# Kernel optimization log

Hardware: AMD Instinct MI355X
Metric: run time of the kernel (lower is better)

Reference implementation:

```python
import jax, jax.numpy as jnp
import numpy as np

T_IN, T_OUT, B, D, H, L = 257, 256, 256, 131, 256, 2


def lstm_cell(x, h, c, Wih, Whh, bih, bhh):
    # torch LSTMCell gate order: i, f, g, o
    z = x @ Wih.T + h @ Whh.T + bih + bhh
    i, f, g, o = jnp.split(z, 4, axis=-1)
    c_new = jax.nn.sigmoid(f) * c + jax.nn.sigmoid(i) * jnp.tanh(g)
    h_new = jax.nn.sigmoid(o) * jnp.tanh(c_new)
    return h_new, c_new


def setup_inputs() -> dict:
    key = jax.random.key(0)
    ks = jax.random.split(key, 22)
    s = 0.05  # weight scale, keeps gates in the linear-ish region
    d = {}
    d["X"] = jax.random.normal(ks[0], (T_IN, B, D), jnp.float32)
    d["Y"] = jax.random.normal(ks[1], (T_OUT, B, D), jnp.float32)
    shapes = {
        "enc_Wih0": (4 * H, D), "enc_Whh0": (4 * H, H), "enc_bih0": (4 * H,), "enc_bhh0": (4 * H,),
        "enc_Wih1": (4 * H, H), "enc_Whh1": (4 * H, H), "enc_bih1": (4 * H,), "enc_bhh1": (4 * H,),
        "dec_Wih0": (4 * H, D), "dec_Whh0": (4 * H, H), "dec_bih0": (4 * H,), "dec_bhh0": (4 * H,),
        "dec_Wih1": (4 * H, H), "dec_Whh1": (4 * H, H), "dec_bih1": (4 * H,), "dec_bhh1": (4 * H,),
        "lin_W": (D, H), "lin_b": (D,),
    }
    for i, (name, shp) in enumerate(shapes.items()):
        d[name] = jax.random.normal(ks[2 + i], shp, jnp.float32) * s
    return d


def _make_step(params, emit):
    def step(carry, x):
        hs, cs = carry
        inp = x
        new_h, new_c = [], []
        for l, (Wih, Whh, bih, bhh) in enumerate(params):
            h, c = lstm_cell(inp, hs[l], cs[l], Wih, Whh, bih, bhh)
            new_h.append(h)
            new_c.append(c)
            inp = h
        out = emit(inp) if emit is not None else None
        return (tuple(new_h), tuple(new_c)), out
    return step


def reference(X, Y, enc_Wih0, enc_Whh0, enc_bih0, enc_bhh0,
              enc_Wih1, enc_Whh1, enc_bih1, enc_bhh1,
              dec_Wih0, dec_Whh0, dec_bih0, dec_bhh0,
              dec_Wih1, dec_Whh1, dec_bih1, dec_bhh1,
              lin_W, lin_b):
    enc = [(enc_Wih0, enc_Whh0, enc_bih0, enc_bhh0),
           (enc_Wih1, enc_Whh1, enc_bih1, enc_bhh1)]
    dec = [(dec_Wih0, dec_Whh0, dec_bih0, dec_bhh0),
           (dec_Wih1, dec_Whh1, dec_bih1, dec_bhh1)]
    b = X.shape[1]
    zeros = tuple(jnp.zeros((b, H), X.dtype) for _ in range(L))
    # encoder over X[:-1]
    (hn, cn), _ = jax.lax.scan(_make_step(enc, None), (zeros, zeros), X[:-1])
    # decoder (teacher forcing): inputs are [X[-1], Y[0], ..., Y[T_out-2]]
    dec_in = jnp.concatenate([X[-1:], Y[:-1]], axis=0)
    emit = lambda h: jax.nn.log_softmax(h @ lin_W.T + lin_b, axis=-1)
    _, Ypred = jax.lax.scan(_make_step(dec, emit), (hn, cn), dec_in)
    return Ypred  # (T_out, B, out_dim) log-probabilities
```

## Files before the change

kernel.cpp:

```cpp
#include <hip/hip_runtime.h>
#include <hip/hip_bf16.h>
#include <math.h>

typedef __attribute__((ext_vector_type(8))) short short8;
typedef __attribute__((ext_vector_type(4))) float f32x4;
typedef unsigned long long u64;
typedef __attribute__((ext_vector_type(2))) unsigned long long u64x2;

#define STEPS 512
#define BB 256
#define HH 256
#define DD 131
#define XP 160
#define K0P 416
#define KS0 424
#define K1  512
#define KS1 520
#define HS0 264
#define HS1 520
#define RING 16
#define PO   8
#define NGRP 8
#define ROWS 32
#define SLOT_E (ROWS * HH)
#define RGELEM (RING * SLOT_E)
#define POISON64 0x7F807F807F807F80ull

#define OFF_W0E 0
#define OFF_W0D (OFF_W0E + 1024 * K0P)
#define OFF_W1E (OFF_W0D + 1024 * K0P)
#define OFF_W1D (OFF_W1E + 1024 * K1)
#define OFF_LW  (OFF_W1D + 1024 * K1)
#define OFF_XBF (OFF_LW + 160 * 256)
#define OFF_H0R (OFF_XBF + (size_t)STEPS * BB * XP)
#define OFF_H1R (OFF_H0R + (size_t)NGRP * RGELEM)
#define OFF_H1A (OFF_H1R + (size_t)NGRP * RGELEM)
#define OFF_BF16_END (OFF_H1A + (size_t)256 * BB * HH)

#define LDS_W_OFF  0
#define LDS_HS_OFF 66560
#define LDS_TOTAL  133120

__device__ __forceinline__ float rcp_(float x) { return __builtin_amdgcn_rcpf(x); }
__device__ __forceinline__ float fsigm(float x) { return rcp_(1.f + __expf(-x)); }
__device__ __forceinline__ float ftanh(float x) {
    float t = __expf(-2.f * fabsf(x));
    float r = (1.f - t) * rcp_(1.f + t);
    return copysignf(r, x);
}
__device__ __forceinline__ void astore(u64* p, u64 v) {
    __hip_atomic_store(p, v, __ATOMIC_RELAXED, __HIP_MEMORY_SCOPE_AGENT);
}
__device__ __forceinline__ void pload(const u64* p, u64x2& r) {
    asm volatile("global_load_dwordx4 %0, %1, off sc0 sc1" : "=v"(r) : "v"(p));
}
__device__ __forceinline__ void pll_drain() {
    asm volatile("s_waitcnt vmcnt(0)" ::: "memory");
    __builtin_amdgcn_sched_barrier(0);
}

__global__ __launch_bounds__(256) void pack_w0(const float* __restrict__ Wih,
                                               const float* __restrict__ Whh,
                                               __hip_bfloat16* __restrict__ dst) {
    int idx = blockIdx.x * 256 + threadIdx.x;
    int p = idx / K0P, k = idx - p * K0P;
    int ct = p >> 6, local = p & 63, g = local >> 4, j = local & 15;
    int orow = g * 256 + ct * 16 + j;
    float v = 0.f;
    if (k < DD) v = Wih[orow * DD + k];
    else if (k >= XP) v = Whh[orow * HH + (k - XP)];
    dst[idx] = __float2bfloat16(v);
}

__global__ __launch_bounds__(256) void pack_w1(const float* __restrict__ Wih,
                                               const float* __restrict__ Whh,
                                               __hip_bfloat16* __restrict__ dst) {
    int idx = blockIdx.x * 256 + threadIdx.x;
    int p = idx >> 9, k = idx & 511;
    int ct = p >> 6, local = p & 63, g = local >> 4, j = local & 15;
    int orow = g * 256 + ct * 16 + j;
    float v = (k < HH) ? Wih[orow * HH + k] : Whh[orow * HH + (k - HH)];
    dst[idx] = __float2bfloat16(v);
}

__global__ __launch_bounds__(256) void pack_bias(const float* __restrict__ bih,
                                                 const float* __restrict__ bhh,
                                                 float* __restrict__ dst) {
    int idx = blockIdx.x * 256 + threadIdx.x;
    if (idx < 1024) dst[idx] = bih[idx] + bhh[idx];
}

__global__ __launch_bounds__(256) void pack_xbf(const float* __restrict__ X,
                                                const float* __restrict__ Y,
                                                __hip_bfloat16* __restrict__ dst) {
    int idx = blockIdx.x * 256 + threadIdx.x;
    int kp = idx % XP;
    int rb = idx / XP;
    int b = rb & 255, s = rb >> 8;
    const float* src;
    if (s <= 256) src = X + ((size_t)s * BB + b) * DD;
    else          src = Y + ((size_t)(s - 257) * BB + b) * DD;
    dst[idx] = __float2bfloat16(kp < DD ? src[kp] : 0.f);
}

__global__ __launch_bounds__(256) void pack_linw(const float* __restrict__ linW,
                                                 __hip_bfloat16* __restrict__ dst) {
    int idx = blockIdx.x * 256 + threadIdx.x;
    int j = idx >> 8, k = idx & 255;
    dst[idx] = __float2bfloat16(j < DD ? linW[j * HH + k] : 0.f);
}

__global__ __launch_bounds__(256) void pack_linb(const float* __restrict__ linb,
                                                 float* __restrict__ dst) {
    int idx = threadIdx.x;
    if (idx < 160) dst[idx] = (idx < DD) ? linb[idx] : -1.0e30f;
}

__global__ __launch_bounds__(256) void init_rings(u64* __restrict__ rings,
                                                  int* __restrict__ acks) {
    int idx = blockIdx.x * 256 + threadIdx.x;
    if (idx < 2 * NGRP * (RGELEM / 4)) {
        int slot = (idx >> 11) & (RING - 1);
        rings[idx] = (slot == RING - 1) ? 0ull : POISON64;
    }
    if (idx < 256) acks[idx] = 0;
}

__global__ __launch_bounds__(512, 1) void lstm_persistent(
    const __hip_bfloat16* __restrict__ wsb,
    const float* __restrict__ bsum,
    __hip_bfloat16* __restrict__ h0ring,
    __hip_bfloat16* __restrict__ h1ring,
    __hip_bfloat16* __restrict__ h1all,
    int* __restrict__ acks) {
    extern __shared__ __align__(16) char lds[];
    __hip_bfloat16* Wlds = (__hip_bfloat16*)(lds + LDS_W_OFF);
    __hip_bfloat16* hst  = (__hip_bfloat16*)(lds + LDS_HS_OFF);

    const int tid = threadIdx.x;
    const int wg = blockIdx.x;
    const int xg = wg >> 5;
    const int slot_id = wg & 31;
    const int layer = slot_id >> 4;
    const int ct = slot_id & 15;
    const int lane = tid & 63;
    const int mt = tid >> 6;
    const int lrow = lane & 15;
    const int lk8 = (lane >> 4) * 8;

    const int K  = layer ? K1 : K0P;
    const int KS = layer ? KS1 : KS0;
    const int HS = layer ? HS1 : HS0;
    int* ackp = acks + xg * 32;

    auto load_w = [&](int ph2) {
        const __hip_bfloat16* src = wsb +
            (layer ? (ph2 ? OFF_W1D : OFF_W1E) : (ph2 ? OFF_W0D : OFF_W0E)) +
            (size_t)ct * 64 * K;
        const int KC = K >> 3;
        for (int e = tid; e < 64 * KC; e += 512) {
            int p = e / KC, kc = e - p * KC;
            *(short8*)&Wlds[p * KS + kc * 8] =
                *(const short8*)&src[(size_t)p * K + kc * 8];
        }
    };
    load_w(0);

    const int jcol = ct * 16 + lrow;
    float br[2][4];
    #pragma unroll
    for (int ph = 0; ph < 2; ++ph)
        #pragma unroll
        for (int g = 0; g < 4; ++g)
            br[ph][g] = bsum[ph * 2048 + layer * 1024 + g * 256 + jcol];
    f32x4 creg = {0.f, 0.f, 0.f, 0.f};

    const __hip_bfloat16* Xbf = wsb + OFF_XBF;
    __hip_bfloat16* h0g = h0ring + (size_t)xg * RGELEM;
    __hip_bfloat16* h1g = h1ring + (size_t)xg * RGELEM;
    __hip_bfloat16* ringw = layer ? h1g : h0g;
    const int arow = mt * 16 + lrow;
    __syncthreads();

    for (int s = 0; s < STEPS; ++s) {
        const int ph = s >> 8;
        const bool defer_x = (s == 256);
        f32x4 acc[4];
        short8 xv[5];

        if (tid < 128) {
            #pragma unroll
            for (int g = 0; g < 4; ++g) acc[g] = (f32x4){0.f, 0.f, 0.f, 0.f};
            if (layer == 0) {
                const short8* xp = (const short8*)
                    &Xbf[((size_t)s * BB + xg * ROWS + arow) * XP];
                #pragma unroll
                for (int kt = 0; kt < 5; ++kt) xv[kt] = xp[kt * 4 + (lk8 >> 3)];
                if (!defer_x) {
                    #pragma unroll
                    for (int kt = 0; kt < 5; ++kt)
                        #pragma unroll
                        for (int g = 0; g < 4; ++g) {
                            short8 w = *(const short8*)
                                &Wlds[(g * 16 + lrow) * KS0 + kt * 32 + lk8];
                            acc[g] = __builtin_amdgcn_mfma_f32_16x16x32_bf16(
                                xv[kt], w, acc[g], 0, 0, 0);
                        }
                }
            }
        } else {
            const int ptid = tid - 128;
            __hip_bfloat16* hs = hst + (s & 1) * 32 * HS;
            if (layer == 0) {
                const u64* src = (const u64*)(h0g +
                    (size_t)((s + RING - 1) & (RING - 1)) * SLOT_E);
                u64x2 v[3];
                unsigned pend = 0;
                #pragma unroll
                for (int i = 0; i < 3; ++i)
                    if (ptid + i * 384 < 1024) pend |= (1u << i);
                int guard = 0;
                while (pend) {
                    #pragma unroll
                    for (int i = 0; i < 3; ++i)
                        if (pend & (1u << i))
                            pload(src + 2 * (ptid + i * 384), v[i]);
                    pll_drain();
                    unsigned np = 0;
                    #pragma unroll
                    for (int i = 0; i < 3; ++i)
                        if ((pend & (1u << i)) &&
                            (((v[i][0] & 0xFFFFull) == 0x7F80ull) ||
                             ((v[i][1] & 0xFFFFull) == 0x7F80ull)))
                            np |= (1u << i);
                    pend = np;
                    if (pend && ++guard > 65536) break;
                }
                #pragma unroll
                for (int i = 0; i < 3; ++i) {
                    int q = ptid + i * 384;
                    if (q < 1024)
                        *(u64x2*)&hs[(q >> 5) * HS0 + (q & 31) * 8] = v[i];
                }
                if (ptid == 383) {
                    int tgt = 16 * (s - (PO - 1));
                    if (tgt > 0) {
                        int guard2 = 0;
                        while (__hip_atomic_load(ackp, __ATOMIC_RELAXED,
                                                 __HIP_MEMORY_SCOPE_AGENT) < tgt) {
                            __builtin_amdgcn_s_sleep(1);
                            if (++guard2 > 65536) break;
                        }
                    }
                }
            } else {
                const u64* s0 = (const u64*)(h0g +
                    (size_t)(s & (RING - 1)) * SLOT_E);
                const u64* s1 = (const u64*)(h1g +
                    (size_t)((s + RING - 1) & (RING - 1)) * SLOT_E);
                u64x2 v0[3], v1[3];
                unsigned pend = 0;
                #pragma unroll
                for (int i = 0; i < 3; ++i)
                    if (ptid + i * 384 < 1024) pend |= (0x101u << i);
                int guard = 0;
                while (pend) {
                    #pragma unroll
                    for (int i = 0; i < 3; ++i) {
                        if (pend & (1u << i))
                            pload(s0 + 2 * (ptid + i * 384), v0[i]);
                        if (pend & (0x100u << i))
                            pload(s1 + 2 * (ptid + i * 384), v1[i]);
                    }
                    pll_drain();
                    unsigned np = 0;
                    #pragma unroll
                    for (int i = 0; i < 3; ++i) {
                        if ((pend & (1u << i)) &&
                            (((v0[i][0] & 0xFFFFull) == 0x7F80ull) ||
                             ((v0[i][1] & 0xFFFFull) == 0x7F80ull)))
                            np |= (1u << i);
                        if ((pend & (0x100u << i)) &&
                            (((v1[i][0] & 0xFFFFull) == 0x7F80ull) ||
                             ((v1[i][1] & 0xFFFFull) == 0x7F80ull)))
                            np |= (0x100u << i);
                    }
                    pend = np;
                    if (pend && ++guard > 65536) break;
                }
                #pragma unroll
                for (int i = 0; i < 3; ++i) {
                    int q = ptid + i * 384;
                    if (q < 1024) {
                        *(u64x2*)&hs[(q >> 5) * HS1 + (q & 31) * 8] = v0[i];
                        *(u64x2*)&hs[(q >> 5) * HS1 + 256 + (q & 31) * 8] = v1[i];
                    }
                }
            }
        }
        __syncthreads();
        if (s == 256) { load_w(1); __syncthreads(); }

        if (tid < 128) {
            if (layer == 1 && tid == 0)
                __hip_atomic_fetch_add(ackp, 1, __ATOMIC_RELAXED,
                                       __HIP_MEMORY_SCOPE_AGENT);
            const __hip_bfloat16* hs = hst + (s & 1) * 32 * HS;
            if (layer == 0) {
                if (defer_x) {
                    #pragma unroll
                    for (int kt = 0; kt < 5; ++kt)
                        #pragma unroll
                        for (int g = 0; g < 4; ++g) {
                            short8 w = *(const short8*)
                                &Wlds[(g * 16 + lrow) * KS0 + kt * 32 + lk8];
                            acc[g] = __builtin_amdgcn_mfma_f32_16x16x32_bf16(
                                xv[kt], w, acc[g], 0, 0, 0);
                        }
                }
                #pragma unroll
                for (int kt = 0; kt < 8; ++kt) {
                    short8 a = *(const short8*)&hs[arow * HS0 + kt * 32 + lk8];
                    #pragma unroll
                    for (int g = 0; g < 4; ++g) {
                        short8 w = *(const short8*)
                            &Wlds[(g * 16 + lrow) * KS0 + (5 + kt) * 32 + lk8];
                        acc[g] = __builtin_amdgcn_mfma_f32_16x16x32_bf16(
                            a, w, acc[g], 0, 0, 0);
                    }
                }
            } else {
                #pragma unroll
                for (int kt = 0; kt < 16; ++kt) {
                    short8 a = *(const short8*)&hs[arow * HS1 + kt * 32 + lk8];
                    #pragma unroll
                    for (int g = 0; g < 4; ++g) {
                        short8 w = *(const short8*)
                            &Wlds[(g * 16 + lrow) * KS1 + kt * 32 + lk8];
                        acc[g] = __builtin_amdgcn_mfma_f32_16x16x32_bf16(
                            a, w, acc[g], 0, 0, 0);
                    }
                }
            }

            unsigned short hu[4];
            #pragma unroll
            for (int r = 0; r < 4; ++r) {
                float zi = acc[0][r] + br[ph][0];
                float zf = acc[1][r] + br[ph][1];
                float zg = acc[2][r] + br[ph][2];
                float zo = acc[3][r] + br[ph][3];
                float ig = fsigm(zi), fg = fsigm(zf), og = fsigm(zo);
                float cn = fg * creg[r] + ig * ftanh(zg);
                creg[r] = cn;
                union { __hip_bfloat16 b; unsigned short u; } cvt;
                cvt.b = __float2bfloat16(og * ftanh(cn));
                hu[r] = cvt.u;
            }

            {
                const int m = lane & 15, g16 = lane >> 4;
                const int srcbase = g16 * 16 + 4 * (m & 3);
                const int myslot = m >> 2;
                unsigned short pa = 0, pb = 0, pc = 0, pd = 0;
                #pragma unroll
                for (int rr = 0; rr < 4; ++rr) {
                    int q0 = __shfl((int)hu[rr], srcbase + 0, 64);
                    int q1 = __shfl((int)hu[rr], srcbase + 1, 64);
                    int q2 = __shfl((int)hu[rr], srcbase + 2, 64);
                    int q3 = __shfl((int)hu[rr], srcbase + 3, 64);
                    if (myslot == rr) {
                        pa = (unsigned short)q0; pb = (unsigned short)q1;
                        pc = (unsigned short)q2; pd = (unsigned short)q3;
                    }
                }
                u64 pkt = (u64)pa | ((u64)pb << 16) | ((u64)pc << 32)
                        | ((u64)pd << 48);
                const int prow = mt * 16 + g16 * 4 + myslot;
                const int pq = m & 3;
                astore((u64*)(ringw + (size_t)(s & (RING - 1)) * SLOT_E)
                       + prow * 64 + ct * 4 + pq, pkt);
                if (layer == 1 && s >= 256)
                    *(u64*)&h1all[((size_t)(s - 256) * BB + xg * ROWS + prow) * HH
                                  + ct * 16 + pq * 4] = pkt;
                astore((u64*)(ringw + (size_t)((s + PO) & (RING - 1)) * SLOT_E)
                       + prow * 64 + ct * 4 + pq, POISON64);
            }
        }
    }
}

__global__ __launch_bounds__(256) void emit_mfma(
    const __hip_bfloat16* __restrict__ h1all,
    const __hip_bfloat16* __restrict__ lW,
    const float* __restrict__ lb,
    float* __restrict__ out) {
    __shared__ float lbs[160];
    const int tid = threadIdx.x;
    const int wv = tid >> 6, lane = tid & 63;
    const int lrow = lane & 15, lk8 = (lane >> 4) * 8, crow = (lane >> 4) * 4;
    const int row0 = blockIdx.x * 64;
    if (tid < 160) lbs[tid] = lb[tid];
    __syncthreads();

    f32x4 acc[10];
    #pragma unroll
    for (int f = 0; f < 10; ++f) acc[f] = (f32x4){0.f, 0.f, 0.f, 0.f};
    const int arow = row0 + wv * 16 + lrow;
    #pragma unroll
    for (int kt = 0; kt < 8; ++kt) {
        short8 a = *reinterpret_cast<const short8*>(
            &h1all[(size_t)arow * HH + kt * 32 + lk8]);
        #pragma unroll
        for (int f = 0; f < 10; ++f) {
            short8 w = *reinterpret_cast<const short8*>(
                &lW[(size_t)(f * 16 + lrow) * HH + kt * 32 + lk8]);
            acc[f] = __builtin_amdgcn_mfma_f32_16x16x32_bf16(a, w, acc[f], 0, 0, 0);
        }
    }
    #pragma unroll
    for (int r = 0; r < 4; ++r) {
        float m = -3.0e38f;
        #pragma unroll
        for (int f = 0; f < 10; ++f) m = fmaxf(m, acc[f][r] + lbs[f * 16 + lrow]);
        #pragma unroll
        for (int d = 1; d < 16; d <<= 1) m = fmaxf(m, __shfl_xor(m, d, 64));
        float ss = 0.f;
        #pragma unroll
        for (int f = 0; f < 10; ++f) ss += __expf(acc[f][r] + lbs[f * 16 + lrow] - m);
        #pragma unroll
        for (int d = 1; d < 16; d <<= 1) ss += __shfl_xor(ss, d, 64);
        float lse = m + logf(ss);
        int grow = row0 + wv * 16 + crow + r;
        #pragma unroll
        for (int f = 0; f < 9; ++f) {
            int j = f * 16 + lrow;
            if (j < DD)
                out[(size_t)grow * DD + j] = acc[f][r] + lbs[j] - lse;
        }
    }
}

extern "C" void kernel_launch(void* const* d_in, const int* in_sizes, int n_in,
                              void* d_out, int out_size, void* d_ws, size_t ws_size,
                              hipStream_t stream) {
    const float* X     = (const float*)d_in[0];
    const float* Y     = (const float*)d_in[1];
    const float* eWih0 = (const float*)d_in[2];
    const float* eWhh0 = (const float*)d_in[3];
    const float* ebih0 = (const float*)d_in[4];
    const float* ebhh0 = (const float*)d_in[5];
    const float* eWih1 = (const float*)d_in[6];
    const float* eWhh1 = (const float*)d_in[7];
    const float* ebih1 = (const float*)d_in[8];
    const float* ebhh1 = (const float*)d_in[9];
    const float* dWih0 = (const float*)d_in[10];
    const float* dWhh0 = (const float*)d_in[11];
    const float* dbih0 = (const float*)d_in[12];
    const float* dbhh0 = (const float*)d_in[13];
    const float* dWih1 = (const float*)d_in[14];
    const float* dWhh1 = (const float*)d_in[15];
    const float* dbih1 = (const float*)d_in[16];
    const float* dbhh1 = (const float*)d_in[17];
    const float* linW  = (const float*)d_in[18];
    const float* linb  = (const float*)d_in[19];
    float* out = (float*)d_out;

    __hip_bfloat16* wsb = (__hip_bfloat16*)d_ws;
    float* freg  = (float*)(wsb + OFF_BF16_END);
    float* bsum  = freg;
    float* linbp = freg + 4096;
    int*   acks  = (int*)(freg + 4096 + 192);

    pack_w0<<<dim3(1664), dim3(256), 0, stream>>>(eWih0, eWhh0, wsb + OFF_W0E);
    pack_w0<<<dim3(1664), dim3(256), 0, stream>>>(dWih0, dWhh0, wsb + OFF_W0D);
    pack_w1<<<dim3(2048), dim3(256), 0, stream>>>(eWih1, eWhh1, wsb + OFF_W1E);
    pack_w1<<<dim3(2048), dim3(256), 0, stream>>>(dWih1, dWhh1, wsb + OFF_W1D);
    pack_bias<<<dim3(4), dim3(256), 0, stream>>>(ebih0, ebhh0, bsum + 0);
    pack_bias<<<dim3(4), dim3(256), 0, stream>>>(ebih1, ebhh1, bsum + 1024);
    pack_bias<<<dim3(4), dim3(256), 0, stream>>>(dbih0, dbhh0, bsum + 2048);
    pack_bias<<<dim3(4), dim3(256), 0, stream>>>(dbih1, dbhh1, bsum + 3072);
    pack_xbf<<<dim3(81920), dim3(256), 0, stream>>>(X, Y, wsb + OFF_XBF);
    pack_linw<<<dim3(160), dim3(256), 0, stream>>>(linW, wsb + OFF_LW);
    pack_linb<<<dim3(1), dim3(256), 0, stream>>>(linb, linbp);
    init_rings<<<dim3(2048), dim3(256), 0, stream>>>((u64*)(wsb + OFF_H0R), acks);

    hipFuncSetAttribute((const void*)lstm_persistent,
                        hipFuncAttributeMaxDynamicSharedMemorySize, LDS_TOTAL);
    lstm_persistent<<<dim3(256), dim3(512), LDS_TOTAL, stream>>>(
        wsb, bsum, wsb + OFF_H0R, wsb + OFF_H1R, wsb + OFF_H1A, acks);

    emit_mfma<<<dim3(1024), dim3(256), 0, stream>>>(wsb + OFF_H1A, wsb + OFF_LW,
                                                    linbp, out);
}
```

Measured before the change: 2.447 ms.

## Drop producer warps and LDS staging; load recurrent h directly into MFMA operands

Removes the 384 producer threads that polled the ring buffers and staged hidden states through LDS, so each of the 128 compute threads now polls its own MFMA A-fragments straight from global memory into registers. The per-step __syncthreads is gone, and the ack counter is split per wave so waves synchronise independently across the pipeline. Layer-0 input-projection MFMAs are issued while the ring loads are in flight. The cost is that polling latency is no longer hidden by separate warps, and workgroups become smaller with more registers per thread.

```diff
diff --git a/kernel.cpp b/kernel.cpp
--- a/kernel.cpp
+++ b/kernel.cpp
@@ -16,8 +16,6 @@
 #define KS0 424
 #define K1  512
 #define KS1 520
-#define HS0 264
-#define HS1 520
 #define RING 16
 #define PO   8
 #define NGRP 8
@@ -37,9 +35,7 @@
 #define OFF_H1A (OFF_H1R + (size_t)NGRP * RGELEM)
 #define OFF_BF16_END (OFF_H1A + (size_t)256 * BB * HH)
 
-#define LDS_W_OFF  0
-#define LDS_HS_OFF 66560
-#define LDS_TOTAL  133120
+#define LDS_TOTAL 66560
 
 __device__ __forceinline__ float rcp_(float x) { return __builtin_amdgcn_rcpf(x); }
 __device__ __forceinline__ float fsigm(float x) { return rcp_(1.f + __expf(-x)); }
@@ -57,6 +53,10 @@
 __device__ __forceinline__ void pll_drain() {
     asm volatile("s_waitcnt vmcnt(0)" ::: "memory");
     __builtin_amdgcn_sched_barrier(0);
+}
+__device__ __forceinline__ bool pois(const u64x2& v) {
+    return ((v[0] & 0xFFFFull) == 0x7F80ull) ||
+           ((v[1] & 0xFFFFull) == 0x7F80ull);
 }
 
 __global__ __launch_bounds__(256) void pack_w0(const float* __restrict__ Wih,
@@ -126,7 +126,7 @@
     if (idx < 256) acks[idx] = 0;
 }
 
-__global__ __launch_bounds__(512, 1) void lstm_persistent(
+__global__ __launch_bounds__(128, 1) void lstm_persistent(
     const __hip_bfloat16* __restrict__ wsb,
     const float* __restrict__ bsum,
     __hip_bfloat16* __restrict__ h0ring,
@@ -134,8 +134,7 @@
     __hip_bfloat16* __restrict__ h1all,
     int* __restrict__ acks) {
     extern __shared__ __align__(16) char lds[];
-    __hip_bfloat16* Wlds = (__hip_bfloat16*)(lds + LDS_W_OFF);
-    __hip_bfloat16* hst  = (__hip_bfloat16*)(lds + LDS_HS_OFF);
+    __hip_bfloat16* Wlds = (__hip_bfloat16*)lds;
 
     const int tid = threadIdx.x;
     const int wg = blockIdx.x;
@@ -150,15 +149,14 @@
 
     const int K  = layer ? K1 : K0P;
     const int KS = layer ? KS1 : KS0;
-    const int HS = layer ? HS1 : HS0;
-    int* ackp = acks + xg * 32;
+    int* ackp = acks + xg * 32 + mt * 8;
 
     auto load_w = [&](int ph2) {
         const __hip_bfloat16* src = wsb +
             (layer ? (ph2 ? OFF_W1D : OFF_W1E) : (ph2 ? OFF_W0D : OFF_W0E)) +
             (size_t)ct * 64 * K;
         const int KC = K >> 3;
-        for (int e = tid; e < 64 * KC; e += 512) {
+        for (int e = tid; e < 64 * KC; e += 128) {
             int p = e / KC, kc = e - p * KC;
             *(short8*)&Wlds[p * KS + kc * 8] =
                 *(const short8*)&src[(size_t)p * K + kc * 8];
@@ -180,213 +178,173 @@
     __hip_bfloat16* h1g = h1ring + (size_t)xg * RGELEM;
     __hip_bfloat16* ringw = layer ? h1g : h0g;
     const int arow = mt * 16 + lrow;
+    const int fb = arow * 64 + (lk8 >> 2);
     __syncthreads();
 
     for (int s = 0; s < STEPS; ++s) {
         const int ph = s >> 8;
-        const bool defer_x = (s == 256);
+        if (s == 256) { __syncthreads(); load_w(1); __syncthreads(); }
+
         f32x4 acc[4];
-        short8 xv[5];
-
-        if (tid < 128) {
-            #pragma unroll
-            for (int g = 0; g < 4; ++g) acc[g] = (f32x4){0.f, 0.f, 0.f, 0.f};
-            if (layer == 0) {
-                const short8* xp = (const short8*)
-                    &Xbf[((size_t)s * BB + xg * ROWS + arow) * XP];
+        #pragma unroll
+        for (int g = 0; g < 4; ++g) acc[g] = (f32x4){0.f, 0.f, 0.f, 0.f};
+
+        if (layer == 0) {
+            if (lane == 63) {
+                int tgt = 16 * (s - (PO - 1));
+                if (tgt > 0) {
+                    int guard = 0;
+                    while (__hip_atomic_load(ackp, __ATOMIC_RELAXED,
+                                             __HIP_MEMORY_SCOPE_AGENT) < tgt) {
+                        __builtin_amdgcn_s_sleep(1);
+                        if (++guard > 65536) break;
+                    }
+                }
+            }
+            const u64* src = (const u64*)(h0g +
+                (size_t)((s + RING - 1) & (RING - 1)) * SLOT_E);
+            u64x2 v[8];
+            #pragma unroll
+            for (int i = 0; i < 8; ++i) pload(src + fb + i * 8, v[i]);
+
+            const short8* xp = (const short8*)
+                &Xbf[((size_t)s * BB + xg * ROWS + arow) * XP];
+            short8 xv[5];
+            #pragma unroll
+            for (int kt = 0; kt < 5; ++kt) xv[kt] = xp[kt * 4 + (lk8 >> 3)];
+            #pragma unroll
+            for (int kt = 0; kt < 5; ++kt)
                 #pragma unroll
-                for (int kt = 0; kt < 5; ++kt) xv[kt] = xp[kt * 4 + (lk8 >> 3)];
-                if (!defer_x) {
-                    #pragma unroll
-                    for (int kt = 0; kt < 5; ++kt)
-                        #pragma unroll
-                        for (int g = 0; g < 4; ++g) {
-                            short8 w = *(const short8*)
-                                &Wlds[(g * 16 + lrow) * KS0 + kt * 32 + lk8];
-                            acc[g] = __builtin_amdgcn_mfma_f32_16x16x32_bf16(
-                                xv[kt], w, acc[g], 0, 0, 0);
-                        }
-                }
-            }
-        } else {
-            const int ptid = tid - 128;
-            __hip_bfloat16* hs = hst + (s & 1) * 32 * HS;
-            if (layer == 0) {
-                const u64* src = (const u64*)(h0g +
-                    (size_t)((s + RING - 1) & (RING - 1)) * SLOT_E);
-                u64x2 v[3];
+                for (int g = 0; g < 4; ++g) {
+                    short8 w = *(const short8*)
+                        &Wlds[(g * 16 + lrow) * KS0 + kt * 32 + lk8];
+                    acc[g] = __builtin_amdgcn_mfma_f32_16x16x32_bf16(
+                        xv[kt], w, acc[g], 0, 0, 0);
+                }
+
+            pll_drain();
+            {
                 unsigned pend = 0;
                 #pragma unroll
-                for (int i = 0; i < 3; ++i)
-                    if (ptid + i * 384 < 1024) pend |= (1u << i);
+                for (int i = 0; i < 8; ++i) if (pois(v[i])) pend |= (1u << i);
                 int guard = 0;
                 while (pend) {
                     #pragma unroll
-                    for (int i = 0; i < 3; ++i)
-                        if (pend & (1u << i))
-                            pload(src + 2 * (ptid + i * 384), v[i]);
+                    for (int i = 0; i < 8; ++i)
+                        if (pend & (1u << i)) pload(src + fb + i * 8, v[i]);
                     pll_drain();
                     unsigned np = 0;
                     #pragma unroll
-                    for (int i = 0; i < 3; ++i)
-                        if ((pend & (1u << i)) &&
-                            (((v[i][0] & 0xFFFFull) == 0x7F80ull) ||
-                             ((v[i][1] & 0xFFFFull) == 0x7F80ull)))
-                            np |= (1u << i);
+                    for (int i = 0; i < 8; ++i)
+                        if ((pend & (1u << i)) && pois(v[i])) np |= (1u << i);
                     pend = np;
                     if (pend && ++guard > 65536) break;
                 }
+            }
+            #pragma unroll
+            for (int kt = 0; kt < 8; ++kt) {
+                union { u64x2 u; short8 s8; } a; a.u = v[kt];
                 #pragma unroll
-                for (int i = 0; i < 3; ++i) {
-                    int q = ptid + i * 384;
-                    if (q < 1024)
-                        *(u64x2*)&hs[(q >> 5) * HS0 + (q & 31) * 8] = v[i];
-                }
-                if (ptid == 383) {
-                    int tgt = 16 * (s - (PO - 1));
-                    if (tgt > 0) {
-                        int guard2 = 0;
-                        while (__hip_atomic_load(ackp, __ATOMIC_RELAXED,
-                                                 __HIP_MEMORY_SCOPE_AGENT) < tgt) {
-                            __builtin_amdgcn_s_sleep(1);
-                            if (++guard2 > 65536) break;
-                        }
-                    }
-                }
-            } else {
-                const u64* s0 = (const u64*)(h0g +
-                    (size_t)(s & (RING - 1)) * SLOT_E);
-                const u64* s1 = (const u64*)(h1g +
-                    (size_t)((s + RING - 1) & (RING - 1)) * SLOT_E);
-                u64x2 v0[3], v1[3];
+                for (int g = 0; g < 4; ++g) {
+                    short8 w = *(const short8*)
+                        &Wlds[(g * 16 + lrow) * KS0 + (5 + kt) * 32 + lk8];
+                    acc[g] = __builtin_amdgcn_mfma_f32_16x16x32_bf16(
+                        a.s8, w, acc[g], 0, 0, 0);
+                }
+            }
+        } else {
+            const u64* s0 = (const u64*)(h0g +
+                (size_t)(s & (RING - 1)) * SLOT_E);
+            const u64* s1 = (const u64*)(h1g +
+                (size_t)((s + RING - 1) & (RING - 1)) * SLOT_E);
+            u64x2 v[16];
+            #pragma unroll
+            for (int i = 0; i < 8; ++i) {
+                pload(s0 + fb + i * 8, v[i]);
+                pload(s1 + fb + i * 8, v[8 + i]);
+            }
+            pll_drain();
+            {
                 unsigned pend = 0;
                 #pragma unroll
-                for (int i = 0; i < 3; ++i)
-                    if (ptid + i * 384 < 1024) pend |= (0x101u << i);
+                for (int i = 0; i < 16; ++i) if (pois(v[i])) pend |= (1u << i);
                 int guard = 0;
                 while (pend) {
                     #pragma unroll
-                    for (int i = 0; i < 3; ++i) {
-                        if (pend & (1u << i))
-                            pload(s0 + 2 * (ptid + i * 384), v0[i]);
-                        if (pend & (0x100u << i))
-                            pload(s1 + 2 * (ptid + i * 384), v1[i]);
-                    }
+                    for (int i = 0; i < 16; ++i)
+                        if (pend & (1u << i)) {
+                            if (i < 8) pload(s0 + fb + i * 8, v[i]);
+                            else       pload(s1 + fb + (i - 8) * 8, v[i]);
+                        }
                     pll_drain();
                     unsigned np = 0;
                     #pragma unroll
-                    for (int i = 0; i < 3; ++i) {
-                        if ((pend & (1u << i)) &&
-                            (((v0[i][0] & 0xFFFFull) == 0x7F80ull) ||
-                             ((v0[i][1] & 0xFFFFull) == 0x7F80ull)))
-                            np |= (1u << i);
-                        if ((pend & (0x100u << i)) &&
-                            (((v1[i][0] & 0xFFFFull) == 0x7F80ull) ||
-                             ((v1[i][1] & 0xFFFFull) == 0x7F80ull)))
-                            np |= (0x100u << i);
-                    }
+                    for (int i = 0; i < 16; ++i)
+                        if ((pend & (1u << i)) && pois(v[i])) np |= (1u << i);
                     pend = np;
                     if (pend && ++guard > 65536) break;
                 }
+            }
+            #pragma unroll
+            for (int kt = 0; kt < 16; ++kt) {
+                union { u64x2 u; short8 s8; } a; a.u = v[kt];
                 #pragma unroll
-                for (int i = 0; i < 3; ++i) {
-                    int q = ptid + i * 384;
-                    if (q < 1024) {
-                        *(u64x2*)&hs[(q >> 5) * HS1 + (q & 31) * 8] = v0[i];
-                        *(u64x2*)&hs[(q >> 5) * HS1 + 256 + (q & 31) * 8] = v1[i];
-                    }
-                }
-            }
-        }
-        __syncthreads();
-        if (s == 256) { load_w(1); __syncthreads(); }
-
-        if (tid < 128) {
-            if (layer == 1 && tid == 0)
-                __hip_atomic_fetch_add(ackp, 1, __ATOMIC_RELAXED,
-                                       __HIP_MEMORY_SCOPE_AGENT);
-            const __hip_bfloat16* hs = hst + (s & 1) * 32 * HS;
-            if (layer == 0) {
-                if (defer_x) {
-                    #pragma unroll
-                    for (int kt = 0; kt < 5; ++kt)
-                        #pragma unroll
-                        for (int g = 0; g < 4; ++g) {
-                            short8 w = *(const short8*)
-                                &Wlds[(g * 16 + lrow) * KS0 + kt * 32 + lk8];
-                            acc[g] = __builtin_amdgcn_mfma_f32_16x16x32_bf16(
-                                xv[kt], w, acc[g], 0, 0, 0);
-                        }
-                }
-                #pragma unroll
-                for (int kt = 0; kt < 8; ++kt) {
-                    short8 a = *(const short8*)&hs[arow * HS0 + kt * 32 + lk8];
-                    #pragma unroll
-                    for (int g = 0; g < 4; ++g) {
-                        short8 w = *(const short8*)
-                            &Wlds[(g * 16 + lrow) * KS0 + (5 + kt) * 32 + lk8];
-                        acc[g] = __builtin_amdgcn_mfma_f32_16x16x32_bf16(
-                            a, w, acc[g], 0, 0, 0);
-                    }
-                }
-            } else {
-                #pragma unroll
-                for (int kt = 0; kt < 16; ++kt) {
-                    short8 a = *(const short8*)&hs[arow * HS1 + kt * 32 + lk8];
-                    #pragma unroll
-                    for (int g = 0; g < 4; ++g) {
-                        short8 w = *(const short8*)
-                            &Wlds[(g * 16 + lrow) * KS1 + kt * 32 + lk8];
-                        acc[g] = __builtin_amdgcn_mfma_f32_16x16x32_bf16(
-                            a, w, acc[g], 0, 0, 0);
-                    }
-                }
-            }
-
-            unsigned short hu[4];
-            #pragma unroll
-            for (int r = 0; r < 4; ++r) {
-                float zi = acc[0][r] + br[ph][0];
-                float zf = acc[1][r] + br[ph][1];
-                float zg = acc[2][r] + br[ph][2];
-                float zo = acc[3][r] + br[ph][3];
-                float ig = fsigm(zi), fg = fsigm(zf), og = fsigm(zo);
-                float cn = fg * creg[r] + ig * ftanh(zg);
-                creg[r] = cn;
-                union { __hip_bfloat16 b; unsigned short u; } cvt;
-                cvt.b = __float2bfloat16(og * ftanh(cn));
-                hu[r] = cvt.u;
-            }
-
-            {
-                const int m = lane & 15, g16 = lane >> 4;
-                const int srcbase = g16 * 16 + 4 * (m & 3);
-                const int myslot = m >> 2;
-                unsigned short pa = 0, pb = 0, pc = 0, pd = 0;
-                #pragma unroll
-                for (int rr = 0; rr < 4; ++rr) {
-                    int q0 = __shfl((int)hu[rr], srcbase + 0, 64);
-                    int q1 = __shfl((int)hu[rr], srcbase + 1, 64);
-                    int q2 = __shfl((int)hu[rr], srcbase + 2, 64);
-                    int q3 = __shfl((int)hu[rr], srcbase + 3, 64);
-                    if (myslot == rr) {
-                        pa = (unsigned short)q0; pb = (unsigned short)q1;
-                        pc = (unsigned short)q2; pd = (unsigned short)q3;
-                    }
-                }
-                u64 pkt = (u64)pa | ((u64)pb << 16) | ((u64)pc << 32)
-                        | ((u64)pd << 48);
-                const int prow = mt * 16 + g16 * 4 + myslot;
-                const int pq = m & 3;
-                astore((u64*)(ringw + (size_t)(s & (RING - 1)) * SLOT_E)
-                       + prow * 64 + ct * 4 + pq, pkt);
-                if (layer == 1 && s >= 256)
-                    *(u64*)&h1all[((size_t)(s - 256) * BB + xg * ROWS + prow) * HH
-                                  + ct * 16 + pq * 4] = pkt;
-                astore((u64*)(ringw + (size_t)((s + PO) & (RING - 1)) * SLOT_E)
-                       + prow * 64 + ct * 4 + pq, POISON64);
-            }
-        }
+                for (int g = 0; g < 4; ++g) {
+                    short8 w = *(const short8*)
+                        &Wlds[(g * 16 + lrow) * KS1 + kt * 32 + lk8];
+                    acc[g] = __builtin_amdgcn_mfma_f32_16x16x32_bf16(
+                        a.s8, w, acc[g], 0, 0, 0);
+                }
+            }
+        }
+
+        unsigned short hu[4];
+        #pragma unroll
+        for (int r = 0; r < 4; ++r) {
+            float zi = acc[0][r] + br[ph][0];
+            float zf = acc[1][r] + br[ph][1];
+            float zg = acc[2][r] + br[ph][2];
+            float zo = acc[3][r] + br[ph][3];
+            float ig = fsigm(zi), fg = fsigm(zf), og = fsigm(zo);
+            float cn = fg * creg[r] + ig * ftanh(zg);
+            creg[r] = cn;
+            union { __hip_bfloat16 b; unsigned short u; } cvt;
+            cvt.b = __float2bfloat16(og * ftanh(cn));
+            hu[r] = cvt.u;
+        }
+
+        {
+            const int m = lane & 15, g16 = lane >> 4;
+            const int srcbase = g16 * 16 + 4 * (m & 3);
+            const int myslot = m >> 2;
+            unsigned short pa = 0, pb = 0, pc = 0, pd = 0;
+            #pragma unroll
+            for (int rr = 0; rr < 4; ++rr) {
+                int q0 = __shfl((int)hu[rr], srcbase + 0, 64);
+                int q1 = __shfl((int)hu[rr], srcbase + 1, 64);
+                int q2 = __shfl((int)hu[rr], srcbase + 2, 64);
+                int q3 = __shfl((int)hu[rr], srcbase + 3, 64);
+                if (myslot == rr) {
+                    pa = (unsigned short)q0; pb = (unsigned short)q1;
+                    pc = (unsigned short)q2; pd = (unsigned short)q3;
+                }
+            }
+            u64 pkt = (u64)pa | ((u64)pb << 16) | ((u64)pc << 32)
+                    | ((u64)pd << 48);
+            const int prow = mt * 16 + g16 * 4 + myslot;
+            const int pq = m & 3;
+            astore((u64*)(ringw + (size_t)(s & (RING - 1)) * SLOT_E)
+                   + prow * 64 + ct * 4 + pq, pkt);
+            if (layer == 1 && s >= 256)
+                *(u64*)&h1all[((size_t)(s - 256) * BB + xg * ROWS + prow) * HH
+                              + ct * 16 + pq * 4] = pkt;
+            astore((u64*)(ringw + (size_t)((s + PO) & (RING - 1)) * SLOT_E)
+                   + prow * 64 + ct * 4 + pq, POISON64);
+        }
+
+        if (layer == 1 && lane == 0)
+            __hip_atomic_fetch_add(ackp, 1, __ATOMIC_RELAXED,
+                                   __HIP_MEMORY_SCOPE_AGENT);
     }
 }
 
@@ -487,7 +445,7 @@
 
     hipFuncSetAttribute((const void*)lstm_persistent,
                         hipFuncAttributeMaxDynamicSharedMemorySize, LDS_TOTAL);
-    lstm_persistent<<<dim3(256), dim3(512), LDS_TOTAL, stream>>>(
+    lstm_persistent<<<dim3(256), dim3(128), LDS_TOTAL, stream>>>(
         wsb, bsum, wsb + OFF_H0R, wsb + OFF_H1R, wsb + OFF_H1A, acks);
 
     emit_mfma<<<dim3(1024), dim3(256), 0, stream>>>(wsb + OFF_H1A, wsb + OFF_LW,
```

Measured after the change: 3.266 ms. 33.5% more time.
